# Kernel optimization log

Measured on AMD Instinct MI355X. Metric: run time of the kernel, lower is better.

## Reference

```python
import jax, jax.numpy as jnp
import numpy as np

E, B = 4, 16384
STATE, ACT, HID = 29, 8, 512
N_POSE, N_LEG = 13, 16

def _leg_inputs(state, act=None):
    # gather per-leg features: for each leg i (stride-2 over 8 joints)
    # [pos_a, vel_a, pos_b, vel_b, (act_a, act_b)] -> concat legs along batch dim
    leg = state[..., -N_LEG:]
    blocks = []
    for i in range(0, 8, 2):
        feats = [leg[..., i], leg[..., 8 + i], leg[..., i + 1], leg[..., 8 + i + 1]]
        if act is not None:
            feats += [act[..., i], act[..., i + 1]]
        blocks.append(jnp.stack(feats, axis=2))
    return jnp.concatenate(blocks, axis=1)  # [E, 4B, 4 or 6]

def _mlp(x, w0, b0, w1, b1, w2, b2, mu, sigma):
    x = (x - mu) / (sigma + 1e-8)
    x = jax.nn.relu(jnp.einsum('ebi,eih->ebh', x, w0) + b0)
    x = jax.nn.relu(jnp.einsum('ebh,ehk->ebk', x, w1) + b1)
    return jnp.einsum('ebh,eho->ebo', x, w2) + b2

def _leg_format(next_legs, b):
    # vectorized form of the original nested-loop scatter in leg_predict
    e = next_legs.shape[0]
    c = next_legs.reshape(e, 4, b, 4).transpose(0, 2, 1, 3)  # [E,B,leg,comp]
    first = jnp.stack([c[..., 0], c[..., 2]], axis=-1).reshape(e, b, 8)   # pos block
    second = jnp.stack([c[..., 1], c[..., 3]], axis=-1).reshape(e, b, 8)  # vel block
    zeros = jnp.zeros((e, b, N_POSE), next_legs.dtype)
    return jnp.concatenate([zeros, first, second], axis=-1)  # [E,B,29]

def reference(state, act, wl0, bl0, wl1, bl1, wl2, bl2, wp0, bp0, wp1, bp1, wp2, bp2,
              mu_leg, sigma_leg, mu_pose, sigma_pose,
              mu_t_leg, sigma_t_leg, mu_t_pose, sigma_t_pose):
    b = state.shape[1]
    out = _mlp(_leg_inputs(state, act), wl0, bl0, wl1, bl1, wl2, bl2, mu_leg, sigma_leg)
    legs_diff = out[..., :4] * (sigma_t_leg + 1e-8) + mu_t_leg          # [E,4B,4] mean head
    legs_curr = _leg_inputs(state)                                       # [E,4B,4]
    next_state_legs = _leg_format(legs_curr + legs_diff, b)              # [E,B,29]
    legs_diff_fmt = _leg_format(legs_diff, b)[..., -N_LEG:]              # [E,B,16]
    pose_in = jnp.concatenate([state[..., :N_POSE], legs_diff_fmt], axis=-1)  # [E,B,29]
    pose = _mlp(pose_in, wp0, bp0, wp1, bp1, wp2, bp2, mu_pose, sigma_pose)[..., :N_POSE]
    pose = pose * (sigma_t_pose + 1e-8) + mu_t_pose + state[..., :N_POSE]
    next_state = jnp.concatenate([pose, next_state_legs[..., N_POSE:]], axis=-1)
    return next_state.mean(0)  # [B, 29]

def setup_inputs():
    key = jax.random.key(0)
    ks = jax.random.split(key, 10)
    s = 0.05
    return {
        'state': jax.random.normal(ks[0], (E, B, STATE), jnp.float32),
        'act': jax.random.normal(ks[1], (E, B, ACT), jnp.float32),
        'wl0': jax.random.normal(ks[2], (E, 6, HID), jnp.float32) * s,
        'bl0': jnp.zeros((E, 1, HID), jnp.float32),
        'wl1': jax.random.normal(ks[3], (E, HID, HID), jnp.float32) * s,
        'bl1': jnp.zeros((E, 1, HID), jnp.float32),
        'wl2': jax.random.normal(ks[4], (E, HID, 8), jnp.float32) * s,
        'bl2': jnp.zeros((E, 1, 8), jnp.float32),
        'wp0': jax.random.normal(ks[5], (E, STATE, HID), jnp.float32) * s,
        'bp0': jnp.zeros((E, 1, HID), jnp.float32),
        'wp1': jax.random.normal(ks[6], (E, HID, HID), jnp.float32) * s,
        'bp1': jnp.zeros((E, 1, HID), jnp.float32),
        'wp2': jax.random.normal(ks[7], (E, HID, 2 * N_POSE), jnp.float32) * s,
        'bp2': jnp.zeros((E, 1, 2 * N_POSE), jnp.float32),
        'mu_leg': jnp.zeros((1, 6), jnp.float32),
        'sigma_leg': jnp.ones((1, 6), jnp.float32),
        'mu_pose': jnp.zeros((1, STATE), jnp.float32),
        'sigma_pose': jnp.ones((1, STATE), jnp.float32),
        'mu_t_leg': jnp.zeros((1, 4), jnp.float32),
        'sigma_t_leg': jnp.ones((1, 4), jnp.float32),
        'mu_t_pose': jnp.zeros((1, N_POSE), jnp.float32),
        'sigma_t_pose': jnp.ones((1, N_POSE), jnp.float32),
    }
```

## Files before the change

### kernel.cpp

```cpp
#include <hip/hip_runtime.h>


#define E_ 4
#define B_ 16384
#define H1S 520
#define H2S 136
#define A0S 40

typedef float f32x4 __attribute__((ext_vector_type(4)));
typedef __bf16 bf16x8 __attribute__((ext_vector_type(8)));

__device__ __forceinline__ f32x4 mfma16(bf16x8 a, bf16x8 b, f32x4 c) {
  return __builtin_amdgcn_mfma_f32_16x16x32_bf16(a, b, c, 0, 0, 0);
}

__device__ __forceinline__ void fmt_map(int k, int& ib, int& j) {
  if (k < 8) { ib = k >> 1; j = (k & 1) ? 2 : 0; }
  else { int k8 = k - 8; ib = k8 >> 1; j = (k8 & 1) ? 3 : 1; }
}

__device__ __forceinline__ void pack_one(int idx, int per_e, int KT, int Kreal,
                                         int Nsrc, int Nval,
                                         const float* __restrict__ src,
                                         const float* __restrict__ sigma,
                                         __bf16* __restrict__ dst)
{
  int e = idx / per_e;
  int rem = idx - e * per_e;
  int g = rem >> 9;
  int nt = g / KT;
  int kt = g - nt * KT;
  int li = rem & 511;
  int lane = li >> 3, j = li & 7;
  int k = kt * 32 + (lane >> 4) * 8 + j;
  int n = nt * 16 + (lane & 15);
  float v = 0.f;
  if (k < Kreal && n < Nval) {
    v = src[(size_t)e * Kreal * Nsrc + (size_t)k * Nsrc + n];
    if (sigma) v *= 1.f / (sigma[k] + 1e-8f);
  }
  dst[idx] = (__bf16)v;
}

__global__ void prep_small(const float* __restrict__ wl0, const float* __restrict__ wl2,
                           const float* __restrict__ wp0, const float* __restrict__ wp2,
                           const float* __restrict__ bl0, const float* __restrict__ bp0,
                           const float* __restrict__ mu_leg, const float* __restrict__ sigma_leg,
                           const float* __restrict__ mu_pose, const float* __restrict__ sigma_pose,
                           __bf16* __restrict__ WL0p, __bf16* __restrict__ WL2p,
                           __bf16* __restrict__ WP0p, __bf16* __restrict__ WP2p,
                           float* __restrict__ bl0f, float* __restrict__ bp0f)
{
  const int S0 = 65536, S2 = 32768;
  const int total = 2 * (S0 + S2) + 4096;
  for (int idx0 = blockIdx.x * blockDim.x + threadIdx.x; idx0 < total;
       idx0 += gridDim.x * blockDim.x) {
    int x = idx0;
    if (x < S0)              { pack_one(x, 16384, 1, 6, 512, 512, wl0, sigma_leg, WL0p); }
    else if ((x -= S0) < S2) { pack_one(x, 8192, 16, 512, 8, 8, wl2, nullptr, WL2p); }
    else if ((x -= S2) < S0) { pack_one(x, 16384, 1, 29, 512, 512, wp0, sigma_pose, WP0p); }
    else if ((x -= S0) < S2) { pack_one(x, 8192, 16, 512, 26, 16, wp2, nullptr, WP2p); }
    else {
      x -= S2;
      if (x < 2048) {
        int e = x >> 9, n = x & 511;
        float s = bl0[e * 512 + n];
        #pragma unroll
        for (int k = 0; k < 6; ++k)
          s -= mu_leg[k] / (sigma_leg[k] + 1e-8f) * wl0[(e * 6 + k) * 512 + n];
        bl0f[e * 512 + n] = s;
      } else {
        x -= 2048;
        int e = x >> 9, n = x & 511;
        float s = bp0[e * 512 + n];
        for (int k = 0; k < 29; ++k)
          s -= mu_pose[k] / (sigma_pose[k] + 1e-8f) * wp0[(e * 29 + k) * 512 + n];
        bp0f[e * 512 + n] = s;
      }
    }
  }
}

__global__ __launch_bounds__(256) void prep_w1(const float* __restrict__ wl1,
                                               const float* __restrict__ wp1,
                                               __bf16* __restrict__ WL1p,
                                               __bf16* __restrict__ WP1p)
{
  __shared__ __bf16 st[512][20];
  const int b = blockIdx.x;
  const float* src = (b & 128) ? wp1 : wl1;
  __bf16* dst = (b & 128) ? WP1p : WL1p;
  const int e = (b >> 5) & 3, nt = b & 31;
  src += (size_t)e * 262144 + nt * 16;
  dst += (size_t)e * 262144 + (size_t)nt * 8192;
  const int t = threadIdx.x;

  const int k0 = t >> 2, nq = t & 3;
  #pragma unroll
  for (int it = 0; it < 8; ++it) {
    int k = it * 64 + k0;
    f32x4 v = *(const f32x4*)(src + (size_t)k * 512 + nq * 4);
    #pragma unroll
    for (int j = 0; j < 4; ++j) st[k][nq * 4 + j] = (__bf16)v[j];
  }
  __syncthreads();
  #pragma unroll
  for (int it = 0; it < 4; ++it) {
    int lo = it * 256 + t;
    int kt = lo >> 6, lane = lo & 63;
    int kb = kt * 32 + (lane >> 4) * 8;
    int n = lane & 15;
    bf16x8 o;
    #pragma unroll
    for (int j = 0; j < 8; ++j) o[j] = st[kb + j][n];
    *(bf16x8*)(dst + (size_t)lo * 8) = o;
  }
}

__global__ __launch_bounds__(512) void fused_kernel(
    const float* __restrict__ state, const float* __restrict__ act,
    const float* __restrict__ bl1, const float* __restrict__ bl2,
    const float* __restrict__ bp1, const float* __restrict__ bp2,
    const float* __restrict__ mu_t_leg, const float* __restrict__ sigma_t_leg,
    const float* __restrict__ mu_t_pose, const float* __restrict__ sigma_t_pose,
    const __bf16* __restrict__ WL0p, const __bf16* __restrict__ WL1p,
    const __bf16* __restrict__ WL2p, const __bf16* __restrict__ WP0p,
    const __bf16* __restrict__ WP1p, const __bf16* __restrict__ WP2p,
    const float* __restrict__ bl0f, const float* __restrict__ bp0f,
    float* __restrict__ out)
{
  __shared__ alignas(16) __bf16 h1[128 * H1S];
  __shared__ alignas(16) __bf16 h2c[64 * H2S];
  __shared__ float ldiff[64][16];
  __shared__ float legacc[64][16];
  __bf16* a0s = h2c;

  const int tid = threadIdx.x;
  const int wv = tid >> 6;
  const int lane = tid & 63;
  const int quad = lane >> 4;
  const int l16 = lane & 15;
  const int b0 = blockIdx.x * 64;

  for (int i = tid; i < 64 * 16; i += 512) ((float*)legacc)[i] = 0.f;
  f32x4 posacc = {0.f, 0.f, 0.f, 0.f};
  __syncthreads();

  for (int e = 0; e < E_; ++e) {
    const float* se = state + (size_t)e * B_ * 29;
    const float* ae = act + (size_t)e * B_ * 8;

    for (int half = 0; half < 2; ++half) {
      __syncthreads();
      for (int i = tid; i < 128 * 32; i += 512) {
        int r = i >> 5, c = i & 31;
        float v = 0.f;
        if (c < 6) {
          int ib = r >> 5;
          int b = b0 + half * 32 + (r & 31);
          const float* sp = se + (size_t)b * 29;
          if (c == 0) v = sp[13 + 2 * ib];
          else if (c == 1) v = sp[21 + 2 * ib];
          else if (c == 2) v = sp[14 + 2 * ib];
          else if (c == 3) v = sp[22 + 2 * ib];
          else if (c == 4) v = ae[(size_t)b * 8 + 2 * ib];
          else v = ae[(size_t)b * 8 + 2 * ib + 1];
        }
        a0s[r * A0S + c] = (__bf16)v;
      }
      __syncthreads();

      {
        const __bf16* W0 = WL0p + (size_t)e * 16384;
        const float* b0v = bl0f + e * 512;
        bf16x8 bfr[4]; float bs[4];
        #pragma unroll
        for (int i = 0; i < 4; ++i) {
          int ct = wv * 4 + i;
          bfr[i] = *(const bf16x8*)(W0 + ((size_t)ct * 64 + lane) * 8);
          bs[i] = b0v[ct * 16 + l16];
        }
        for (int rt = 0; rt < 8; ++rt) {
          bf16x8 afr = *(const bf16x8*)&a0s[(rt * 16 + l16) * A0S + quad * 8];
          #pragma unroll
          for (int i = 0; i < 4; ++i) {
            f32x4 acc = {bs[i], bs[i], bs[i], bs[i]};
            acc = mfma16(afr, bfr[i], acc);
            int col = (wv * 4 + i) * 16 + l16;
            #pragma unroll
            for (int r = 0; r < 4; ++r)
              h1[(rt * 16 + quad * 4 + r) * H1S + col] = (__bf16)fmaxf(acc[r], 0.f);
          }
        }
      }
      __syncthreads();

      const __bf16* W1 = WL1p + (size_t)e * 262144;
      const __bf16* W2 = WL2p + (size_t)e * 8192;
      const float* b1v = bl1 + e * 512;
      const int rg = wv >> 2, cg = wv & 3;
      float bv2 = (l16 < 8) ? bl2[e * 8 + l16] : 0.f;
      f32x4 oacc = {bv2, bv2, bv2, bv2};

      for (int cc = 0; cc < 4; ++cc) {
        f32x4 acc[4][2];
        #pragma unroll
        for (int ct = 0; ct < 2; ++ct) {
          float bias = b1v[cc * 128 + cg * 32 + ct * 16 + l16];
          #pragma unroll
          for (int i = 0; i < 4; ++i) acc[i][ct] = (f32x4){bias, bias, bias, bias};
        }
        const __bf16* Wc = W1 + (size_t)(cc * 8 + cg * 2) * 8192;
        #pragma unroll 4
        for (int kt = 0; kt < 16; ++kt) {
          bf16x8 afr[4];
          #pragma unroll
          for (int i = 0; i < 4; ++i)
            afr[i] = *(const bf16x8*)&h1[(rg * 64 + i * 16 + l16) * H1S + kt * 32 + quad * 8];
          #pragma unroll
          for (int ct = 0; ct < 2; ++ct) {
            bf16x8 bfr = *(const bf16x8*)(Wc + (((size_t)ct * 16 + kt) * 64 + lane) * 8);
            #pragma unroll
            for (int i = 0; i < 4; ++i) acc[i][ct] = mfma16(afr[i], bfr, acc[i][ct]);
          }
        }
        #pragma unroll
        for (int hh = 0; hh < 2; ++hh) {
          __syncthreads();
          if (rg == hh) {
            #pragma unroll
            for (int i = 0; i < 4; ++i)
              #pragma unroll
              for (int ct = 0; ct < 2; ++ct)
                #pragma unroll
                for (int r = 0; r < 4; ++r)
                  h2c[(i * 16 + quad * 4 + r) * H2S + cg * 32 + ct * 16 + l16] =
                      (__bf16)fmaxf(acc[i][ct][r], 0.f);
          }
          __syncthreads();
          if ((wv >> 2) == hh) {
            #pragma unroll
            for (int k2 = 0; k2 < 4; ++k2) {
              bf16x8 afr2 = *(const bf16x8*)&h2c[((wv & 3) * 16 + l16) * H2S + k2 * 32 + quad * 8];
              bf16x8 bfr2 = *(const bf16x8*)(W2 + ((size_t)(cc * 4 + k2) * 64 + lane) * 8);
              oacc = mfma16(afr2, bfr2, oacc);
            }
          }
        }
      }
      if (l16 < 4) {
        float sc = sigma_t_leg[l16] + 1e-8f;
        float mv = mu_t_leg[l16];
        #pragma unroll
        for (int r = 0; r < 4; ++r) {
          int L = wv * 16 + quad * 4 + r;
          ldiff[half * 32 + (L & 31)][(L >> 5) * 4 + l16] = oacc[r] * sc + mv;
        }
      }
    }

    __syncthreads();
    for (int i = tid; i < 64 * 32; i += 512) {
      int t = i >> 5, c = i & 31;
      float v = 0.f;
      if (c < 13) v = se[(size_t)(b0 + t) * 29 + c];
      else if (c < 29) { int ib, j; fmt_map(c - 13, ib, j); v = ldiff[t][ib * 4 + j]; }
      a0s[t * A0S + c] = (__bf16)v;
    }
    for (int i = tid; i < 64 * 16; i += 512) {
      int t = i >> 4, k = i & 15;
      int ib, j; fmt_map(k, ib, j);
      legacc[t][k] += se[(size_t)(b0 + t) * 29 + 13 + k] + ldiff[t][ib * 4 + j];
    }
    __syncthreads();

    {
      const __bf16* W0 = WP0p + (size_t)e * 16384;
      const float* b0v = bp0f + e * 512;
      bf16x8 bfr[4]; float bs[4];
      #pragma unroll
      for (int i = 0; i < 4; ++i) {
        int ct = wv * 4 + i;
        bfr[i] = *(const bf16x8*)(W0 + ((size_t)ct * 64 + lane) * 8);
        bs[i] = b0v[ct * 16 + l16];
      }
      for (int rt = 0; rt < 4; ++rt) {
        bf16x8 afr = *(const bf16x8*)&a0s[(rt * 16 + l16) * A0S + quad * 8];
        #pragma unroll
        for (int i = 0; i < 4; ++i) {
          f32x4 acc = {bs[i], bs[i], bs[i], bs[i]};
          acc = mfma16(afr, bfr[i], acc);
          int col = (wv * 4 + i) * 16 + l16;
          #pragma unroll
          for (int r = 0; r < 4; ++r)
            h1[(rt * 16 + quad * 4 + r) * H1S + col] = (__bf16)fmaxf(acc[r], 0.f);
        }
      }
    }
    __syncthreads();

    {
      const __bf16* W1 = WP1p + (size_t)e * 262144;
      const __bf16* W2 = WP2p + (size_t)e * 8192;
      const float* b1v = bp1 + e * 512;
      float bvp = bp2[e * 26 + l16];
      f32x4 po = {bvp, bvp, bvp, bvp};

      for (int cc2 = 0; cc2 < 2; ++cc2) {
        f32x4 acc[4][2];
        #pragma unroll
        for (int ct = 0; ct < 2; ++ct) {
          float bias = b1v[cc2 * 256 + wv * 32 + ct * 16 + l16];
          #pragma unroll
          for (int i = 0; i < 4; ++i) acc[i][ct] = (f32x4){bias, bias, bias, bias};
        }
        const __bf16* Wc = W1 + (size_t)(cc2 * 16 + wv * 2) * 8192;
        #pragma unroll 4
        for (int kt = 0; kt < 16; ++kt) {
          bf16x8 afr[4];
          #pragma unroll
          for (int i = 0; i < 4; ++i)
            afr[i] = *(const bf16x8*)&h1[(i * 16 + l16) * H1S + kt * 32 + quad * 8];
          #pragma unroll
          for (int ct = 0; ct < 2; ++ct) {
            bf16x8 bfr = *(const bf16x8*)(Wc + (((size_t)ct * 16 + kt) * 64 + lane) * 8);
            #pragma unroll
            for (int i = 0; i < 4; ++i) acc[i][ct] = mfma16(afr[i], bfr, acc[i][ct]);
          }
        }
        #pragma unroll
        for (int hh = 0; hh < 2; ++hh) {
          __syncthreads();
          if ((wv >> 2) == hh) {
            int cgl = wv & 3;
            #pragma unroll
            for (int i = 0; i < 4; ++i)
              #pragma unroll
              for (int ct = 0; ct < 2; ++ct)
                #pragma unroll
                for (int r = 0; r < 4; ++r)
                  h2c[(i * 16 + quad * 4 + r) * H2S + cgl * 32 + ct * 16 + l16] =
                      (__bf16)fmaxf(acc[i][ct][r], 0.f);
          }
          __syncthreads();
          if (wv < 4) {
            #pragma unroll
            for (int k2 = 0; k2 < 4; ++k2) {
              bf16x8 afr2 = *(const bf16x8*)&h2c[(wv * 16 + l16) * H2S + k2 * 32 + quad * 8];
              bf16x8 bfr2 = *(const bf16x8*)(W2 + ((size_t)(cc2 * 8 + hh * 4 + k2) * 64 + lane) * 8);
              po = mfma16(afr2, bfr2, po);
            }
          }
        }
      }
      if (wv < 4 && l16 < 13) {
        float sc = sigma_t_pose[l16] + 1e-8f;
        float mv = mu_t_pose[l16];
        #pragma unroll
        for (int r = 0; r < 4; ++r) {
          int row = wv * 16 + quad * 4 + r;
          posacc[r] += po[r] * sc + mv + se[(size_t)(b0 + row) * 29 + l16];
        }
      }
    }
  }

  if (wv < 4 && l16 < 13) {
    #pragma unroll
    for (int r = 0; r < 4; ++r) {
      int row = wv * 16 + quad * 4 + r;
      out[(size_t)(b0 + row) * 29 + l16] = 0.25f * posacc[r];
    }
  }
  for (int i = tid; i < 64 * 16; i += 512) {
    int t = i >> 4, k = i & 15;
    out[(size_t)(b0 + t) * 29 + 13 + k] = 0.25f * legacc[t][k];
  }
}

extern "C" void kernel_launch(void* const* d_in, const int* in_sizes, int n_in,
                              void* d_out, int out_size, void* d_ws, size_t ws_size,
                              hipStream_t stream) {
  const float* state = (const float*)d_in[0];
  const float* act = (const float*)d_in[1];
  const float* wl0 = (const float*)d_in[2];
  const float* bl0 = (const float*)d_in[3];
  const float* wl1 = (const float*)d_in[4];
  const float* bl1 = (const float*)d_in[5];
  const float* wl2 = (const float*)d_in[6];
  const float* bl2 = (const float*)d_in[7];
  const float* wp0 = (const float*)d_in[8];
  const float* bp0 = (const float*)d_in[9];
  const float* wp1 = (const float*)d_in[10];
  const float* bp1 = (const float*)d_in[11];
  const float* wp2 = (const float*)d_in[12];
  const float* bp2 = (const float*)d_in[13];
  const float* mu_leg = (const float*)d_in[14];
  const float* sigma_leg = (const float*)d_in[15];
  const float* mu_pose = (const float*)d_in[16];
  const float* sigma_pose = (const float*)d_in[17];
  const float* mu_t_leg = (const float*)d_in[18];
  const float* sigma_t_leg = (const float*)d_in[19];
  const float* mu_t_pose = (const float*)d_in[20];
  const float* sigma_t_pose = (const float*)d_in[21];
  float* out = (float*)d_out;

  char* ws = (char*)d_ws;
  __bf16* WL0p = (__bf16*)(ws);
  __bf16* WL1p = (__bf16*)(ws + 131072);
  __bf16* WL2p = (__bf16*)(ws + 2228224);
  __bf16* WP0p = (__bf16*)(ws + 2293760);
  __bf16* WP1p = (__bf16*)(ws + 2424832);
  __bf16* WP2p = (__bf16*)(ws + 4521984);
  float* bl0f = (float*)(ws + 4587520);
  float* bp0f = (float*)(ws + 4595712);

  prep_small<<<256, 256, 0, stream>>>(wl0, wl2, wp0, wp2, bl0, bp0,
                                      mu_leg, sigma_leg, mu_pose, sigma_pose,
                                      WL0p, WL2p, WP0p, WP2p, bl0f, bp0f);
  prep_w1<<<256, 256, 0, stream>>>(wl1, wp1, WL1p, WP1p);
  fused_kernel<<<256, 512, 0, stream>>>(state, act, bl1, bl2, bp1, bp2,
                                        mu_t_leg, sigma_t_leg, mu_t_pose, sigma_t_pose,
                                        WL0p, WL1p, WL2p, WP0p, WP1p, WP2p,
                                        bl0f, bp0f, out);
}
```

Before: 365.2 us.

## Replace leg output-layer MFMA staging with register FMA and shuffle reduction

The leg MLP's final 512x4 projection no longer stages relu'd hidden activations through shared memory with two barriers per column chunk. Each lane now multiplies its accumulator values by fp32 output weights read from global memory, keeps partial sums in registers, reduces them across the 16-lane column group with xor shuffles, and adds the results into the leg-diff buffer with shared atomics. The bias and denormalisation are moved to the consumer loops. The goal is to remove barriers and LDS traffic, at the cost of more VALU work, 64 extra accumulator registers, and atomic contention.

```diff
diff --git a/kernel.cpp b/kernel.cpp
--- a/kernel.cpp
+++ b/kernel.cpp
@@ -119,13 +119,14 @@
 
 __global__ __launch_bounds__(512) void fused_kernel(
     const float* __restrict__ state, const float* __restrict__ act,
+    const float* __restrict__ wl2,
     const float* __restrict__ bl1, const float* __restrict__ bl2,
     const float* __restrict__ bp1, const float* __restrict__ bp2,
     const float* __restrict__ mu_t_leg, const float* __restrict__ sigma_t_leg,
     const float* __restrict__ mu_t_pose, const float* __restrict__ sigma_t_pose,
     const __bf16* __restrict__ WL0p, const __bf16* __restrict__ WL1p,
-    const __bf16* __restrict__ WL2p, const __bf16* __restrict__ WP0p,
-    const __bf16* __restrict__ WP1p, const __bf16* __restrict__ WP2p,
+    const __bf16* __restrict__ WP0p, const __bf16* __restrict__ WP1p,
+    const __bf16* __restrict__ WP2p,
     const float* __restrict__ bl0f, const float* __restrict__ bp0f,
     float* __restrict__ out)
 {
@@ -149,6 +150,9 @@
   for (int e = 0; e < E_; ++e) {
     const float* se = state + (size_t)e * B_ * 29;
     const float* ae = act + (size_t)e * B_ * 8;
+    const float* w2e = wl2 + (size_t)e * 4096;
+
+    for (int i = tid; i < 64 * 16; i += 512) ((float*)ldiff)[i] = 0.f;
 
     for (int half = 0; half < 2; ++half) {
       __syncthreads();
@@ -196,11 +200,13 @@
       __syncthreads();
 
       const __bf16* W1 = WL1p + (size_t)e * 262144;
-      const __bf16* W2 = WL2p + (size_t)e * 8192;
       const float* b1v = bl1 + e * 512;
       const int rg = wv >> 2, cg = wv & 3;
-      float bv2 = (l16 < 8) ? bl2[e * 8 + l16] : 0.f;
-      f32x4 oacc = {bv2, bv2, bv2, bv2};
+      f32x4 preg[4][4];
+      #pragma unroll
+      for (int i = 0; i < 4; ++i)
+        #pragma unroll
+        for (int r = 0; r < 4; ++r) preg[i][r] = (f32x4){0.f, 0.f, 0.f, 0.f};
 
       for (int cc = 0; cc < 4; ++cc) {
         f32x4 acc[4][2];
@@ -225,38 +231,38 @@
           }
         }
         #pragma unroll
-        for (int hh = 0; hh < 2; ++hh) {
-          __syncthreads();
-          if (rg == hh) {
-            #pragma unroll
-            for (int i = 0; i < 4; ++i)
-              #pragma unroll
-              for (int ct = 0; ct < 2; ++ct)
-                #pragma unroll
-                for (int r = 0; r < 4; ++r)
-                  h2c[(i * 16 + quad * 4 + r) * H2S + cg * 32 + ct * 16 + l16] =
-                      (__bf16)fmaxf(acc[i][ct][r], 0.f);
-          }
-          __syncthreads();
-          if ((wv >> 2) == hh) {
-            #pragma unroll
-            for (int k2 = 0; k2 < 4; ++k2) {
-              bf16x8 afr2 = *(const bf16x8*)&h2c[((wv & 3) * 16 + l16) * H2S + k2 * 32 + quad * 8];
-              bf16x8 bfr2 = *(const bf16x8*)(W2 + ((size_t)(cc * 4 + k2) * 64 + lane) * 8);
-              oacc = mfma16(afr2, bfr2, oacc);
-            }
-          }
-        }
-      }
-      if (l16 < 4) {
-        float sc = sigma_t_leg[l16] + 1e-8f;
-        float mv = mu_t_leg[l16];
+        for (int ct = 0; ct < 2; ++ct) {
+          int col = cc * 128 + cg * 32 + ct * 16 + l16;
+          f32x4 w2v = *(const f32x4*)(w2e + col * 8);
+          #pragma unroll
+          for (int i = 0; i < 4; ++i)
+            #pragma unroll
+            for (int r = 0; r < 4; ++r)
+              preg[i][r] += w2v * fmaxf(acc[i][ct][r], 0.f);
+        }
+      }
+      #pragma unroll
+      for (int i = 0; i < 4; ++i)
         #pragma unroll
         for (int r = 0; r < 4; ++r) {
-          int L = wv * 16 + quad * 4 + r;
-          ldiff[half * 32 + (L & 31)][(L >> 5) * 4 + l16] = oacc[r] * sc + mv;
-        }
-      }
+          f32x4 p = preg[i][r];
+          #pragma unroll
+          for (int c = 0; c < 4; ++c) {
+            p[c] += __shfl_xor(p[c], 1);
+            p[c] += __shfl_xor(p[c], 2);
+            p[c] += __shfl_xor(p[c], 4);
+            p[c] += __shfl_xor(p[c], 8);
+          }
+          if (l16 == i * 4 + r) {
+            int L = rg * 64 + i * 16 + quad * 4 + r;
+            int t = half * 32 + (L & 31);
+            int ib4 = (L >> 5) * 4;
+            atomicAdd(&ldiff[t][ib4 + 0], p[0]);
+            atomicAdd(&ldiff[t][ib4 + 1], p[1]);
+            atomicAdd(&ldiff[t][ib4 + 2], p[2]);
+            atomicAdd(&ldiff[t][ib4 + 3], p[3]);
+          }
+        }
     }
 
     __syncthreads();
@@ -264,13 +270,19 @@
       int t = i >> 5, c = i & 31;
       float v = 0.f;
       if (c < 13) v = se[(size_t)(b0 + t) * 29 + c];
-      else if (c < 29) { int ib, j; fmt_map(c - 13, ib, j); v = ldiff[t][ib * 4 + j]; }
+      else if (c < 29) {
+        int ib, j; fmt_map(c - 13, ib, j);
+        v = (ldiff[t][ib * 4 + j] + bl2[e * 8 + j]) * (sigma_t_leg[j] + 1e-8f)
+            + mu_t_leg[j];
+      }
       a0s[t * A0S + c] = (__bf16)v;
     }
     for (int i = tid; i < 64 * 16; i += 512) {
       int t = i >> 4, k = i & 15;
       int ib, j; fmt_map(k, ib, j);
-      legacc[t][k] += se[(size_t)(b0 + t) * 29 + 13 + k] + ldiff[t][ib * 4 + j];
+      float d = (ldiff[t][ib * 4 + j] + bl2[e * 8 + j]) * (sigma_t_leg[j] + 1e-8f)
+                + mu_t_leg[j];
+      legacc[t][k] += se[(size_t)(b0 + t) * 29 + 13 + k] + d;
     }
     __syncthreads();
 
@@ -419,8 +431,8 @@
                                       mu_leg, sigma_leg, mu_pose, sigma_pose,
                                       WL0p, WL2p, WP0p, WP2p, bl0f, bp0f);
   prep_w1<<<256, 256, 0, stream>>>(wl1, wp1, WL1p, WP1p);
-  fused_kernel<<<256, 512, 0, stream>>>(state, act, bl1, bl2, bp1, bp2,
+  fused_kernel<<<256, 512, 0, stream>>>(state, act, wl2, bl1, bl2, bp1, bp2,
                                         mu_t_leg, sigma_t_leg, mu_t_pose, sigma_t_pose,
-                                        WL0p, WL1p, WL2p, WP0p, WP1p, WP2p,
+                                        WL0p, WL1p, WP0p, WP1p, WP2p,
                                         bl0f, bp0f, out);
 }
```

Result: slower. 485.8 us (+33.0%).

## Batch pose MLP over ensemble pairs so all waves work on 128 rows

Applied to the files above, without the earlier changes.

Groups ensemble members in pairs and runs the pose MLP for both members together. The hidden layer covers 128 rows, and each half of the workgroup's waves handles one member's 64 rows with its own weights. Before, the pose hidden-2 and output stages used 64 rows per member, and only half the waves did the output MFMAs. The change is meant to raise MFMA utilisation and halve the number of barrier-heavy pose passes. The cost is a second ldiff buffer in LDS and a final cross-wave reduction of the pose accumulators through shared memory.

```diff
diff --git a/kernel.cpp b/kernel.cpp
--- a/kernel.cpp
+++ b/kernel.cpp
@@ -131,7 +131,8 @@
 {
   __shared__ alignas(16) __bf16 h1[128 * H1S];
   __shared__ alignas(16) __bf16 h2c[64 * H2S];
-  __shared__ float ldiff[64][16];
+  __shared__ float ldiffA[64][16];
+  __shared__ float ldiffB[64][16];
   __shared__ float legacc[64][16];
   __bf16* a0s = h2c;
 
@@ -141,140 +142,154 @@
   const int quad = lane >> 4;
   const int l16 = lane & 15;
   const int b0 = blockIdx.x * 64;
+  const int rg = wv >> 2, cg = wv & 3;
 
   for (int i = tid; i < 64 * 16; i += 512) ((float*)legacc)[i] = 0.f;
   f32x4 posacc = {0.f, 0.f, 0.f, 0.f};
   __syncthreads();
 
-  for (int e = 0; e < E_; ++e) {
-    const float* se = state + (size_t)e * B_ * 29;
-    const float* ae = act + (size_t)e * B_ * 8;
-
-    for (int half = 0; half < 2; ++half) {
-      __syncthreads();
-      for (int i = tid; i < 128 * 32; i += 512) {
-        int r = i >> 5, c = i & 31;
-        float v = 0.f;
-        if (c < 6) {
-          int ib = r >> 5;
-          int b = b0 + half * 32 + (r & 31);
-          const float* sp = se + (size_t)b * 29;
-          if (c == 0) v = sp[13 + 2 * ib];
-          else if (c == 1) v = sp[21 + 2 * ib];
-          else if (c == 2) v = sp[14 + 2 * ib];
-          else if (c == 3) v = sp[22 + 2 * ib];
-          else if (c == 4) v = ae[(size_t)b * 8 + 2 * ib];
-          else v = ae[(size_t)b * 8 + 2 * ib + 1];
-        }
-        a0s[r * A0S + c] = (__bf16)v;
-      }
-      __syncthreads();
-
-      {
-        const __bf16* W0 = WL0p + (size_t)e * 16384;
-        const float* b0v = bl0f + e * 512;
-        bf16x8 bfr[4]; float bs[4];
-        #pragma unroll
-        for (int i = 0; i < 4; ++i) {
-          int ct = wv * 4 + i;
-          bfr[i] = *(const bf16x8*)(W0 + ((size_t)ct * 64 + lane) * 8);
-          bs[i] = b0v[ct * 16 + l16];
-        }
-        for (int rt = 0; rt < 8; ++rt) {
-          bf16x8 afr = *(const bf16x8*)&a0s[(rt * 16 + l16) * A0S + quad * 8];
+  for (int p = 0; p < 2; ++p) {
+    const float* se0 = state + (size_t)(2 * p) * B_ * 29;
+    const float* se1 = state + (size_t)(2 * p + 1) * B_ * 29;
+
+    for (int eh = 0; eh < 2; ++eh) {
+      const int e = 2 * p + eh;
+      const float* se = eh ? se1 : se0;
+      const float* ae = act + (size_t)e * B_ * 8;
+      float (*ldif)[16] = eh ? ldiffB : ldiffA;
+
+      for (int half = 0; half < 2; ++half) {
+        __syncthreads();
+        for (int i = tid; i < 128 * 32; i += 512) {
+          int r = i >> 5, c = i & 31;
+          float v = 0.f;
+          if (c < 6) {
+            int ib = r >> 5;
+            int b = b0 + half * 32 + (r & 31);
+            const float* sp = se + (size_t)b * 29;
+            if (c == 0) v = sp[13 + 2 * ib];
+            else if (c == 1) v = sp[21 + 2 * ib];
+            else if (c == 2) v = sp[14 + 2 * ib];
+            else if (c == 3) v = sp[22 + 2 * ib];
+            else if (c == 4) v = ae[(size_t)b * 8 + 2 * ib];
+            else v = ae[(size_t)b * 8 + 2 * ib + 1];
+          }
+          a0s[r * A0S + c] = (__bf16)v;
+        }
+        __syncthreads();
+
+        {
+          const __bf16* W0 = WL0p + (size_t)e * 16384;
+          const float* b0v = bl0f + e * 512;
+          bf16x8 bfr[4]; float bs[4];
           #pragma unroll
           for (int i = 0; i < 4; ++i) {
-            f32x4 acc = {bs[i], bs[i], bs[i], bs[i]};
-            acc = mfma16(afr, bfr[i], acc);
-            int col = (wv * 4 + i) * 16 + l16;
-            #pragma unroll
-            for (int r = 0; r < 4; ++r)
-              h1[(rt * 16 + quad * 4 + r) * H1S + col] = (__bf16)fmaxf(acc[r], 0.f);
-          }
-        }
-      }
-      __syncthreads();
-
-      const __bf16* W1 = WL1p + (size_t)e * 262144;
-      const __bf16* W2 = WL2p + (size_t)e * 8192;
-      const float* b1v = bl1 + e * 512;
-      const int rg = wv >> 2, cg = wv & 3;
-      float bv2 = (l16 < 8) ? bl2[e * 8 + l16] : 0.f;
-      f32x4 oacc = {bv2, bv2, bv2, bv2};
-
-      for (int cc = 0; cc < 4; ++cc) {
-        f32x4 acc[4][2];
-        #pragma unroll
-        for (int ct = 0; ct < 2; ++ct) {
-          float bias = b1v[cc * 128 + cg * 32 + ct * 16 + l16];
-          #pragma unroll
-          for (int i = 0; i < 4; ++i) acc[i][ct] = (f32x4){bias, bias, bias, bias};
-        }
-        const __bf16* Wc = W1 + (size_t)(cc * 8 + cg * 2) * 8192;
-        #pragma unroll 4
-        for (int kt = 0; kt < 16; ++kt) {
-          bf16x8 afr[4];
-          #pragma unroll
-          for (int i = 0; i < 4; ++i)
-            afr[i] = *(const bf16x8*)&h1[(rg * 64 + i * 16 + l16) * H1S + kt * 32 + quad * 8];
+            int ct = wv * 4 + i;
+            bfr[i] = *(const bf16x8*)(W0 + ((size_t)ct * 64 + lane) * 8);
+            bs[i] = b0v[ct * 16 + l16];
+          }
+          for (int rt = 0; rt < 8; ++rt) {
+            bf16x8 afr = *(const bf16x8*)&a0s[(rt * 16 + l16) * A0S + quad * 8];
+            #pragma unroll
+            for (int i = 0; i < 4; ++i) {
+              f32x4 acc = {bs[i], bs[i], bs[i], bs[i]};
+              acc = mfma16(afr, bfr[i], acc);
+              int col = (wv * 4 + i) * 16 + l16;
+              #pragma unroll
+              for (int r = 0; r < 4; ++r)
+                h1[(rt * 16 + quad * 4 + r) * H1S + col] = (__bf16)fmaxf(acc[r], 0.f);
+            }
+          }
+        }
+        __syncthreads();
+
+        const __bf16* W1 = WL1p + (size_t)e * 262144;
+        const __bf16* W2 = WL2p + (size_t)e * 8192;
+        const float* b1v = bl1 + e * 512;
+        float bv2 = (l16 < 8) ? bl2[e * 8 + l16] : 0.f;
+        f32x4 oacc = {bv2, bv2, bv2, bv2};
+
+        for (int cc = 0; cc < 4; ++cc) {
+          f32x4 acc[4][2];
           #pragma unroll
           for (int ct = 0; ct < 2; ++ct) {
-            bf16x8 bfr = *(const bf16x8*)(Wc + (((size_t)ct * 16 + kt) * 64 + lane) * 8);
-            #pragma unroll
-            for (int i = 0; i < 4; ++i) acc[i][ct] = mfma16(afr[i], bfr, acc[i][ct]);
-          }
-        }
-        #pragma unroll
-        for (int hh = 0; hh < 2; ++hh) {
-          __syncthreads();
-          if (rg == hh) {
+            float bias = b1v[cc * 128 + cg * 32 + ct * 16 + l16];
+            #pragma unroll
+            for (int i = 0; i < 4; ++i) acc[i][ct] = (f32x4){bias, bias, bias, bias};
+          }
+          const __bf16* Wc = W1 + (size_t)(cc * 8 + cg * 2) * 8192;
+          #pragma unroll 4
+          for (int kt = 0; kt < 16; ++kt) {
+            bf16x8 afr[4];
             #pragma unroll
             for (int i = 0; i < 4; ++i)
+              afr[i] = *(const bf16x8*)&h1[(rg * 64 + i * 16 + l16) * H1S + kt * 32 + quad * 8];
+            #pragma unroll
+            for (int ct = 0; ct < 2; ++ct) {
+              bf16x8 bfr = *(const bf16x8*)(Wc + (((size_t)ct * 16 + kt) * 64 + lane) * 8);
               #pragma unroll
-              for (int ct = 0; ct < 2; ++ct)
+              for (int i = 0; i < 4; ++i) acc[i][ct] = mfma16(afr[i], bfr, acc[i][ct]);
+            }
+          }
+          #pragma unroll
+          for (int hh = 0; hh < 2; ++hh) {
+            __syncthreads();
+            if (rg == hh) {
+              #pragma unroll
+              for (int i = 0; i < 4; ++i)
                 #pragma unroll
-                for (int r = 0; r < 4; ++r)
-                  h2c[(i * 16 + quad * 4 + r) * H2S + cg * 32 + ct * 16 + l16] =
-                      (__bf16)fmaxf(acc[i][ct][r], 0.f);
-          }
-          __syncthreads();
-          if ((wv >> 2) == hh) {
-            #pragma unroll
-            for (int k2 = 0; k2 < 4; ++k2) {
-              bf16x8 afr2 = *(const bf16x8*)&h2c[((wv & 3) * 16 + l16) * H2S + k2 * 32 + quad * 8];
-              bf16x8 bfr2 = *(const bf16x8*)(W2 + ((size_t)(cc * 4 + k2) * 64 + lane) * 8);
-              oacc = mfma16(afr2, bfr2, oacc);
+                for (int ct = 0; ct < 2; ++ct)
+                  #pragma unroll
+                  for (int r = 0; r < 4; ++r)
+                    h2c[(i * 16 + quad * 4 + r) * H2S + cg * 32 + ct * 16 + l16] =
+                        (__bf16)fmaxf(acc[i][ct][r], 0.f);
             }
-          }
-        }
-      }
-      if (l16 < 4) {
-        float sc = sigma_t_leg[l16] + 1e-8f;
-        float mv = mu_t_leg[l16];
-        #pragma unroll
-        for (int r = 0; r < 4; ++r) {
-          int L = wv * 16 + quad * 4 + r;
-          ldiff[half * 32 + (L & 31)][(L >> 5) * 4 + l16] = oacc[r] * sc + mv;
+            __syncthreads();
+            if ((wv >> 2) == hh) {
+              #pragma unroll
+              for (int k2 = 0; k2 < 4; ++k2) {
+                bf16x8 afr2 = *(const bf16x8*)&h2c[((wv & 3) * 16 + l16) * H2S + k2 * 32 + quad * 8];
+                bf16x8 bfr2 = *(const bf16x8*)(W2 + ((size_t)(cc * 4 + k2) * 64 + lane) * 8);
+                oacc = mfma16(afr2, bfr2, oacc);
+              }
+            }
+          }
+        }
+        if (l16 < 4) {
+          float sc = sigma_t_leg[l16] + 1e-8f;
+          float mv = mu_t_leg[l16];
+          #pragma unroll
+          for (int r = 0; r < 4; ++r) {
+            int L = wv * 16 + quad * 4 + r;
+            ldif[half * 32 + (L & 31)][(L >> 5) * 4 + l16] = oacc[r] * sc + mv;
+          }
         }
       }
     }
 
     __syncthreads();
-    for (int i = tid; i < 64 * 32; i += 512) {
-      int t = i >> 5, c = i & 31;
+    for (int i = tid; i < 128 * 32; i += 512) {
+      int r = i >> 5, c = i & 31;
+      int eh = r >> 6, t = r & 63;
+      const float* se = eh ? se1 : se0;
+      float (*ldif)[16] = eh ? ldiffB : ldiffA;
       float v = 0.f;
       if (c < 13) v = se[(size_t)(b0 + t) * 29 + c];
-      else if (c < 29) { int ib, j; fmt_map(c - 13, ib, j); v = ldiff[t][ib * 4 + j]; }
-      a0s[t * A0S + c] = (__bf16)v;
-    }
-    for (int i = tid; i < 64 * 16; i += 512) {
-      int t = i >> 4, k = i & 15;
+      else if (c < 29) { int ib, j; fmt_map(c - 13, ib, j); v = ldif[t][ib * 4 + j]; }
+      a0s[r * A0S + c] = (__bf16)v;
+    }
+    for (int i = tid; i < 2 * 64 * 16; i += 512) {
+      int eh = i >> 10, i2 = i & 1023;
+      int t = i2 >> 4, k = i2 & 15;
+      const float* se = eh ? se1 : se0;
+      float (*ldif)[16] = eh ? ldiffB : ldiffA;
       int ib, j; fmt_map(k, ib, j);
-      legacc[t][k] += se[(size_t)(b0 + t) * 29 + 13 + k] + ldiff[t][ib * 4 + j];
+      legacc[t][k] += se[(size_t)(b0 + t) * 29 + 13 + k] + ldif[t][ib * 4 + j];
     }
     __syncthreads();
 
-    {
+    for (int eh = 0; eh < 2; ++eh) {
+      const int e = 2 * p + eh;
       const __bf16* W0 = WP0p + (size_t)e * 16384;
       const float* b0v = bp0f + e * 512;
       bf16x8 bfr[4]; float bs[4];
@@ -284,7 +299,7 @@
         bfr[i] = *(const bf16x8*)(W0 + ((size_t)ct * 64 + lane) * 8);
         bs[i] = b0v[ct * 16 + l16];
       }
-      for (int rt = 0; rt < 4; ++rt) {
+      for (int rt = eh * 4; rt < eh * 4 + 4; ++rt) {
         bf16x8 afr = *(const bf16x8*)&a0s[(rt * 16 + l16) * A0S + quad * 8];
         #pragma unroll
         for (int i = 0; i < 4; ++i) {
@@ -300,27 +315,28 @@
     __syncthreads();
 
     {
-      const __bf16* W1 = WP1p + (size_t)e * 262144;
-      const __bf16* W2 = WP2p + (size_t)e * 8192;
-      const float* b1v = bp1 + e * 512;
-      float bvp = bp2[e * 26 + l16];
+      const int epw = 2 * p + rg;
+      const __bf16* W1 = WP1p + (size_t)epw * 262144;
+      const __bf16* W2 = WP2p + (size_t)epw * 8192;
+      const float* b1v = bp1 + epw * 512;
+      float bvp = bp2[epw * 26 + l16];
       f32x4 po = {bvp, bvp, bvp, bvp};
 
-      for (int cc2 = 0; cc2 < 2; ++cc2) {
+      for (int cc = 0; cc < 4; ++cc) {
         f32x4 acc[4][2];
         #pragma unroll
         for (int ct = 0; ct < 2; ++ct) {
-          float bias = b1v[cc2 * 256 + wv * 32 + ct * 16 + l16];
+          float bias = b1v[cc * 128 + cg * 32 + ct * 16 + l16];
           #pragma unroll
           for (int i = 0; i < 4; ++i) acc[i][ct] = (f32x4){bias, bias, bias, bias};
         }
-        const __bf16* Wc = W1 + (size_t)(cc2 * 16 + wv * 2) * 8192;
+        const __bf16* Wc = W1 + (size_t)(cc * 8 + cg * 2) * 8192;
         #pragma unroll 4
         for (int kt = 0; kt < 16; ++kt) {
           bf16x8 afr[4];
           #pragma unroll
           for (int i = 0; i < 4; ++i)
-            afr[i] = *(const bf16x8*)&h1[(i * 16 + l16) * H1S + kt * 32 + quad * 8];
+            afr[i] = *(const bf16x8*)&h1[(rg * 64 + i * 16 + l16) * H1S + kt * 32 + quad * 8];
           #pragma unroll
           for (int ct = 0; ct < 2; ++ct) {
             bf16x8 bfr = *(const bf16x8*)(Wc + (((size_t)ct * 16 + kt) * 64 + lane) * 8);
@@ -331,45 +347,52 @@
         #pragma unroll
         for (int hh = 0; hh < 2; ++hh) {
           __syncthreads();
-          if ((wv >> 2) == hh) {
-            int cgl = wv & 3;
+          if (rg == hh) {
             #pragma unroll
             for (int i = 0; i < 4; ++i)
               #pragma unroll
               for (int ct = 0; ct < 2; ++ct)
                 #pragma unroll
                 for (int r = 0; r < 4; ++r)
-                  h2c[(i * 16 + quad * 4 + r) * H2S + cgl * 32 + ct * 16 + l16] =
+                  h2c[(i * 16 + quad * 4 + r) * H2S + cg * 32 + ct * 16 + l16] =
                       (__bf16)fmaxf(acc[i][ct][r], 0.f);
           }
           __syncthreads();
-          if (wv < 4) {
+          if ((wv >> 2) == hh) {
             #pragma unroll
             for (int k2 = 0; k2 < 4; ++k2) {
-              bf16x8 afr2 = *(const bf16x8*)&h2c[(wv * 16 + l16) * H2S + k2 * 32 + quad * 8];
-              bf16x8 bfr2 = *(const bf16x8*)(W2 + ((size_t)(cc2 * 8 + hh * 4 + k2) * 64 + lane) * 8);
+              bf16x8 afr2 = *(const bf16x8*)&h2c[((wv & 3) * 16 + l16) * H2S + k2 * 32 + quad * 8];
+              bf16x8 bfr2 = *(const bf16x8*)(W2 + ((size_t)(cc * 4 + k2) * 64 + lane) * 8);
               po = mfma16(afr2, bfr2, po);
             }
           }
         }
       }
-      if (wv < 4 && l16 < 13) {
+      if (l16 < 13) {
+        const float* se = rg ? se1 : se0;
         float sc = sigma_t_pose[l16] + 1e-8f;
         float mv = mu_t_pose[l16];
         #pragma unroll
         for (int r = 0; r < 4; ++r) {
-          int row = wv * 16 + quad * 4 + r;
+          int row = (wv & 3) * 16 + quad * 4 + r;
           posacc[r] += po[r] * sc + mv + se[(size_t)(b0 + row) * 29 + l16];
         }
       }
     }
   }
 
+  __syncthreads();
+  if (wv >= 4 && l16 < 13) {
+    #pragma unroll
+    for (int r = 0; r < 4; ++r)
+      ldiffA[(wv & 3) * 16 + quad * 4 + r][l16] = posacc[r];
+  }
+  __syncthreads();
   if (wv < 4 && l16 < 13) {
     #pragma unroll
     for (int r = 0; r < 4; ++r) {
       int row = wv * 16 + quad * 4 + r;
-      out[(size_t)(b0 + row) * 29 + l16] = 0.25f * posacc[r];
+      out[(size_t)(b0 + row) * 29 + l16] = 0.25f * (posacc[r] + ldiffA[row][l16]);
     }
   }
   for (int i = tid; i < 64 * 16; i += 512) {
```

Result: slower. 375.8 us (+2.9%).
